# Kernel tuning notes

Hardware: AMD Instinct MI355X
Metric: run time of the kernel (lower is better)

The kernel has to match this reference:

```python
import jax, jax.numpy as jnp
import numpy as np

N_ROWS = 8192
EMBED_DIM = 256


def setup_inputs() -> dict:
    key = jax.random.key(0)
    k1, k2, k3, k4, k5 = jax.random.split(key, 5)
    M = jax.random.normal(k1, (N_ROWS, EMBED_DIM), dtype=jnp.float32)
    N = jax.random.normal(k2, (N_ROWS, EMBED_DIM), dtype=jnp.float32)
    # gate_w: nn.Linear(embed_dim, 1) -> weight [1, d], bias [1]; gate_b extra scalar param [1]
    Wg = jax.random.normal(k3, (1, EMBED_DIM), dtype=jnp.float32) * 0.06
    bg = jax.random.normal(k4, (1,), dtype=jnp.float32) * 0.1
    gate_b = jax.random.normal(k5, (1,), dtype=jnp.float32) * 0.1
    return {"M": M, "N": N, "Wg": Wg, "bg": bg, "gate_b": gate_b, "iseval": 0}


def reference(M, N, Wg, bg, gate_b, iseval):
    # mt: [n, n] cross-similarity scores
    mt = jnp.matmul(N, M.T)
    if not iseval:
        # training branch: zero out the diagonal (mt - diag(diag(mt)))
        n = mt.shape[0]
        idx = jnp.arange(n)
        mt = mt.at[idx, idx].set(0.0)
    else:
        # eval branch: zero out the first row
        mt = mt.at[0].set(0.0)
    attn_weight = jax.nn.softmax(mt, axis=-1)          # [n, n]
    out_attn = jnp.matmul(attn_weight, M)              # [n, d]
    gate = jax.nn.sigmoid(jnp.matmul(out_attn, Wg.T) + bg + gate_b)  # [n, 1]
    boosted = out_attn * gate + N * (1.0 - gate)       # [n, d]
    return boosted[:, None, None, :]                   # [n, 1, 1, d]
```

## Files before the change

### kernel.cpp

```cpp
#include <hip/hip_runtime.h>


constexpr int EMBED = 256;
constexpr int BQ = 64;
constexpr int BJ = 32;
constexpr int NT = 256;

constexpr int SS_OFF = 0;
constexpr int SS_BUF = 18432;
constexpr int PH_OFF = 36864;
constexpr int PH_BUF = 5120;
constexpr int MS_OFF = 47104;
constexpr int LS_OFF = 47360;
constexpr int AS_OFF = 47616;
constexpr int AS_BUF = 256;
constexpr int LDS_SZ = 48128;

typedef _Float16 half8 __attribute__((ext_vector_type(8)));
typedef float f32x4 __attribute__((ext_vector_type(4)));
typedef short short8v __attribute__((ext_vector_type(8)));

static __device__ __forceinline__ f32x4 mfma16(half8 a, half8 b, f32x4 c) {
    return __builtin_amdgcn_mfma_f32_16x16x32_f16(a, b, c, 0, 0, 0);
}
static __device__ __forceinline__ short f2h(float x) {
    return (short)__builtin_bit_cast(unsigned short, (_Float16)x);
}

__global__ void prep(const float* __restrict__ M,
                     short* __restrict__ MhG, short* __restrict__ MtG) {
    __shared__ float L[16 * 260];
    const int r0 = blockIdx.x * 16;
    const int t = threadIdx.x;
    const int pj = t >> 4, pc = (t & 15) * 16;
    {
        const float* src = M + (size_t)(r0 + pj) * EMBED + pc;
        float4 v[4];
        #pragma unroll
        for (int i = 0; i < 4; ++i) v[i] = ((const float4*)src)[i];
        short* hd = MhG + (size_t)(r0 + pj) * EMBED + pc;
        #pragma unroll
        for (int i = 0; i < 2; ++i) {
            float4 a = v[2 * i], b = v[2 * i + 1];
            short8v h;
            h[0]=f2h(a.x); h[1]=f2h(a.y); h[2]=f2h(a.z); h[3]=f2h(a.w);
            h[4]=f2h(b.x); h[5]=f2h(b.y); h[6]=f2h(b.z); h[7]=f2h(b.w);
            *(short8v*)(hd + 8 * i) = h;
        }
        #pragma unroll
        for (int i = 0; i < 4; ++i)
            *(float4*)(L + pj * 260 + pc + 4 * i) = v[i];
    }
    __syncthreads();
    {
        const int d = t;
        const int tile = r0 >> 5, jh = (r0 >> 4) & 1;
        short* dst = MtG + (size_t)tile * (BJ * EMBED) + d * BJ + jh * 16;
        #pragma unroll
        for (int g2 = 0; g2 < 2; ++g2) {
            short8v w;
            #pragma unroll
            for (int e = 0; e < 8; ++e) w[e] = f2h(L[(g2 * 8 + e) * 260 + d]);
            *(short8v*)(dst + g2 * 8) = w;
        }
    }
}

__launch_bounds__(NT, 2)
__global__ void attn(const short* __restrict__ MhG, const short* __restrict__ MtG,
                     const float* __restrict__ Ng, const int* __restrict__ iseval_p,
                     float* __restrict__ O0out, short* __restrict__ Ofp,
                     float* __restrict__ MLm, float* __restrict__ MLl, int n)
{
    __shared__ __align__(16) char smem[LDS_SZ];
    float* MS = (float*)(smem + MS_OFF);
    float* LS = (float*)(smem + LS_OFF);

    const int t = threadIdx.x, lane = t & 63, wave = t >> 6;
    const int quad = lane >> 4, mn = lane & 15;
    const int bid = blockIdx.x;
    const int s  = (bid & 7) >> 1;
    const int qb = ((bid >> 3) << 1) | (bid & 1);
    const int q0 = qb * BQ;
    const int jbase = s * (n >> 2);
    const int jb32 = jbase / BJ;
    const int ntiles = (n >> 2) / BJ;
    const int iseval = *iseval_p;
    const int jt = wave & 1, kh = wave >> 1;
    const int dq = wave;
    const int sq = t >> 2, sh = t & 3;

    if (t < BQ) { MS[t] = -1e30f; LS[t] = 0.f; }

    half8 Qf[4][4];
    #pragma unroll
    for (int qi = 0; qi < 4; ++qi) {
        const float* np = Ng + (size_t)(q0 + qi * 16 + mn) * EMBED;
        #pragma unroll
        for (int kk = 0; kk < 4; ++kk) {
            const float* p = np + (kh * 4 + kk) * 32 + quad * 8;
            float4 a = *(const float4*)p, b = *(const float4*)(p + 4);
            half8 h;
            h[0]=(_Float16)a.x; h[1]=(_Float16)a.y; h[2]=(_Float16)a.z; h[3]=(_Float16)a.w;
            h[4]=(_Float16)b.x; h[5]=(_Float16)b.y; h[6]=(_Float16)b.z; h[7]=(_Float16)b.w;
            Qf[qi][kk] = h;
        }
    }

    f32x4 O[4][4];
    #pragma unroll
    for (int qi = 0; qi < 4; ++qi)
        #pragma unroll
        for (int dt = 0; dt < 4; ++dt) O[qi][dt] = (f32x4){0.f, 0.f, 0.f, 0.f};

    const short* mhb0 = MhG + (size_t)(jbase + jt * 16 + mn) * EMBED + kh * 128 + quad * 8;
    half8 Bc[4], Bn[4], Mtf[4];
    #pragma unroll
    for (int kk = 0; kk < 4; ++kk) Bc[kk] = *(const half8*)(mhb0 + kk * 32);

    for (int tt = 0; tt <= ntiles; ++tt) {
        const int bw = tt & 1;
        const int br = bw ^ 1;

        if (tt > 0) {
            const short* mtb = MtG + (size_t)(jb32 + (tt - 1)) * (BJ * EMBED);
            #pragma unroll
            for (int dt = 0; dt < 4; ++dt)
                Mtf[dt] = *(const half8*)(mtb + (dq * 64 + dt * 16 + mn) * BJ + quad * 8);
        }

        if (tt < ntiles) {
            f32x4 a0 = (f32x4){0,0,0,0}, a1 = (f32x4){0,0,0,0};
            f32x4 a2 = (f32x4){0,0,0,0}, a3 = (f32x4){0,0,0,0};
            #pragma unroll
            for (int kk = 0; kk < 4; ++kk) {
                half8 bf = Bc[kk];
                a0 = mfma16(Qf[0][kk], bf, a0);
                a1 = mfma16(Qf[1][kk], bf, a1);
                a2 = mfma16(Qf[2][kk], bf, a2);
                a3 = mfma16(Qf[3][kk], bf, a3);
            }
            float* ssp = (float*)(smem + SS_OFF + bw * SS_BUF) + kh * 2304;
            #pragma unroll
            for (int r = 0; r < 4; ++r) {
                ssp[(0  + quad * 4 + r) * 36 + jt * 16 + mn] = a0[r];
                ssp[(16 + quad * 4 + r) * 36 + jt * 16 + mn] = a1[r];
                ssp[(32 + quad * 4 + r) * 36 + jt * 16 + mn] = a2[r];
                ssp[(48 + quad * 4 + r) * 36 + jt * 16 + mn] = a3[r];
            }
        }

        if (tt + 1 < ntiles) {
            const short* nb = mhb0 + (size_t)(tt + 1) * (BJ * EMBED);
            #pragma unroll
            for (int kk = 0; kk < 4; ++kk) Bn[kk] = *(const half8*)(nb + kk * 32);
        }

        if (tt > 0) {
            const int j0g = jbase + (tt - 1) * BJ;
            const float* p0 = (const float*)(smem + SS_OFF + br * SS_BUF) + sq * 36 + 8 * sh;
            float4 sa = *(const float4*)p0;
            float4 sb = *(const float4*)(p0 + 4);
            float4 sc = *(const float4*)(p0 + 2304);
            float4 sd = *(const float4*)(p0 + 2308);
            float sv[8] = {sa.x + sc.x, sa.y + sc.y, sa.z + sc.z, sa.w + sc.w,
                           sb.x + sd.x, sb.y + sd.y, sb.z + sd.z, sb.w + sd.w};
            const int qg = q0 + sq;
            if (iseval) {
                if (qg == 0) {
                    #pragma unroll
                    for (int i = 0; i < 8; ++i) sv[i] = 0.f;
                }
            } else {
                int dj = qg - j0g - 8 * sh;
                #pragma unroll
                for (int i = 0; i < 8; ++i) if (dj == i) sv[i] = 0.f;
            }
            float mx = sv[0];
            #pragma unroll
            for (int i = 1; i < 8; ++i) mx = fmaxf(mx, sv[i]);
            mx = fmaxf(mx, __shfl_xor(mx, 1));
            mx = fmaxf(mx, __shfl_xor(mx, 2));
            float m_old = MS[sq];
            float m_new = fmaxf(m_old, mx);
            float alpha = __expf(m_old - m_new);
            float p[8], ps = 0.f;
            #pragma unroll
            for (int i = 0; i < 8; ++i) { p[i] = __expf(sv[i] - m_new); ps += p[i]; }
            ps += __shfl_xor(ps, 1);
            ps += __shfl_xor(ps, 2);
            if (sh == 0) {
                MS[sq] = m_new;
                ((float*)(smem + AS_OFF + br * AS_BUF))[sq] = alpha;
                LS[sq] = LS[sq] * alpha + ps;
            }
            half8 ph;
            #pragma unroll
            for (int i = 0; i < 8; ++i) ph[i] = (_Float16)p[i];
            *(half8*)(smem + PH_OFF + br * PH_BUF + sq * 80 + sh * 16) = ph;
        }

        __syncthreads();

        if (tt > 0) {
            #pragma unroll
            for (int qi = 0; qi < 4; ++qi) {
                half8 pf = *(const half8*)(smem + PH_OFF + br * PH_BUF + (qi * 16 + mn) * 80 + quad * 16);
                f32x4 al = *(const f32x4*)((const float*)(smem + AS_OFF + br * AS_BUF) + qi * 16 + quad * 4);
                #pragma unroll
                for (int dt = 0; dt < 4; ++dt) {
                    f32x4 o = O[qi][dt];
                    o[0] *= al[0]; o[1] *= al[1]; o[2] *= al[2]; o[3] *= al[3];
                    O[qi][dt] = mfma16(pf, Mtf[dt], o);
                }
            }
        }

        #pragma unroll
        for (int kk = 0; kk < 4; ++kk) Bc[kk] = Bn[kk];
    }

    if (s == 0) {
        #pragma unroll
        for (int qi = 0; qi < 4; ++qi)
            #pragma unroll
            for (int dt = 0; dt < 4; ++dt) {
                int col = dq * 64 + dt * 16 + mn;
                #pragma unroll
                for (int r = 0; r < 4; ++r)
                    O0out[(size_t)(q0 + qi * 16 + quad * 4 + r) * EMBED + col] = O[qi][dt][r];
            }
    } else {
        short* dst = Ofp + (size_t)(s - 1) * n * EMBED;
        #pragma unroll
        for (int qi = 0; qi < 4; ++qi)
            #pragma unroll
            for (int dt = 0; dt < 4; ++dt) {
                int col = dq * 64 + dt * 16 + mn;
                #pragma unroll
                for (int r = 0; r < 4; ++r)
                    dst[(size_t)(q0 + qi * 16 + quad * 4 + r) * EMBED + col] = f2h(O[qi][dt][r]);
            }
    }
    if (t < BQ) {
        MLm[s * n + q0 + t] = MS[t];
        MLl[s * n + q0 + t] = LS[t];
    }
}

__global__ void combine4(const float* __restrict__ O0, const short* __restrict__ Ofp,
                         const float* __restrict__ MLm, const float* __restrict__ MLl,
                         const float* __restrict__ Ng, const float* __restrict__ Wg,
                         const float* __restrict__ bg, const float* __restrict__ gb,
                         float* __restrict__ out, int n)
{
    const int t = threadIdx.x;
    const int row = blockIdx.x * 16 + (t >> 4);
    const int c = t & 15;
    float ms[4], ls[4];
    #pragma unroll
    for (int k = 0; k < 4; ++k) { ms[k] = MLm[k * n + row]; ls[k] = MLl[k * n + row]; }
    float m = fmaxf(fmaxf(ms[0], ms[1]), fmaxf(ms[2], ms[3]));
    float w[4], lsum = 0.f;
    #pragma unroll
    for (int k = 0; k < 4; ++k) { w[k] = __expf(ms[k] - m); lsum += w[k] * ls[k]; }
    float linv = 1.f / lsum;

    float acc[16];
    {
        const float4* o0 = (const float4*)(O0 + (size_t)row * EMBED + c * 16);
        #pragma unroll
        for (int i = 0; i < 4; ++i) {
            float4 v = o0[i];
            acc[4*i+0] = w[0] * v.x; acc[4*i+1] = w[0] * v.y;
            acc[4*i+2] = w[0] * v.z; acc[4*i+3] = w[0] * v.w;
        }
    }
    #pragma unroll
    for (int k = 1; k < 4; ++k) {
        const short* op = Ofp + (size_t)(k - 1) * n * EMBED + (size_t)row * EMBED + c * 16;
        half8 a = *(const half8*)op, b = *(const half8*)(op + 8);
        #pragma unroll
        for (int i = 0; i < 8; ++i) {
            acc[i]     += w[k] * (float)a[i];
            acc[8 + i] += w[k] * (float)b[i];
        }
    }
    float dot = 0.f;
    #pragma unroll
    for (int i = 0; i < 16; ++i) { acc[i] *= linv; dot += acc[i] * Wg[c * 16 + i]; }
    dot += __shfl_xor(dot, 1);
    dot += __shfl_xor(dot, 2);
    dot += __shfl_xor(dot, 4);
    dot += __shfl_xor(dot, 8);
    float g = 1.f / (1.f + __expf(-(dot + bg[0] + gb[0])));
    const float4* n4 = (const float4*)(Ng + (size_t)row * EMBED + c * 16);
    float4* o4 = (float4*)(out + (size_t)row * EMBED + c * 16);
    #pragma unroll
    for (int i = 0; i < 4; ++i) {
        float4 nn = n4[i];
        float4 res;
        res.x = acc[4*i+0] * g + nn.x * (1.f - g);
        res.y = acc[4*i+1] * g + nn.y * (1.f - g);
        res.z = acc[4*i+2] * g + nn.z * (1.f - g);
        res.w = acc[4*i+3] * g + nn.w * (1.f - g);
        o4[i] = res;
    }
}

extern "C" void kernel_launch(void* const* d_in, const int* in_sizes, int n_in,
                              void* d_out, int out_size, void* d_ws, size_t ws_size,
                              hipStream_t stream) {
    const float* M      = (const float*)d_in[0];
    const float* N      = (const float*)d_in[1];
    const float* Wgp    = (const float*)d_in[2];
    const float* bgp    = (const float*)d_in[3];
    const float* gbp    = (const float*)d_in[4];
    const int*   iseval = (const int*)d_in[5];
    float* out = (float*)d_out;

    int n = in_sizes[0] / EMBED;
    short* MhG = (short*)d_ws;
    short* MtG = MhG + (size_t)n * EMBED;
    short* Ofp = MtG + (size_t)n * EMBED;
    float* MLm = (float*)(Ofp + (size_t)3 * n * EMBED);
    float* MLl = MLm + 4 * n;

    hipLaunchKernelGGL(prep, dim3(n / 16), dim3(NT), 0, stream, M, MhG, MtG);
    hipLaunchKernelGGL(attn, dim3((n / BQ) * 4), dim3(NT), 0, stream,
                       MhG, MtG, N, iseval, out, Ofp, MLm, MLl, n);
    hipLaunchKernelGGL(combine4, dim3(n / 16), dim3(NT), 0, stream,
                       out, Ofp, MLm, MLl, N, Wgp, bgp, gbp, out, n);
}
```

Measured before the change: 185.3 us.

## Split QK^T across query halves instead of K halves, keep softmax stats in registers

Each wave now computes full-K dot products for half of the query rows (2 q-tiles × 8 k-chunks) instead of half the K dimension for all 4 q-tiles. This removes the partial-sum buffer and the second pair of LDS reads and adds in the softmax stage, halving the score scratch in LDS. Running max and sum move from LDS into per-thread registers, which drops shared-memory traffic and the sh==0 stores. The trade-off is more B-fragment registers per wave (8 half8 for Bc/Bn plus 16 for Qf), which may raise register pressure against the two-blocks-per-SIMD launch bound.

After: 240.4 us. 1.3x slower.

```diff
diff --git a/kernel.cpp b/kernel.cpp
--- a/kernel.cpp
+++ b/kernel.cpp
@@ -7,14 +7,12 @@
 constexpr int NT = 256;
 
 constexpr int SS_OFF = 0;
-constexpr int SS_BUF = 18432;
-constexpr int PH_OFF = 36864;
+constexpr int SS_BUF = 9216;
+constexpr int PH_OFF = 18432;
 constexpr int PH_BUF = 5120;
-constexpr int MS_OFF = 47104;
-constexpr int LS_OFF = 47360;
-constexpr int AS_OFF = 47616;
+constexpr int AS_OFF = 28672;
 constexpr int AS_BUF = 256;
-constexpr int LDS_SZ = 48128;
+constexpr int LDS_SZ = 29184;
 
 typedef _Float16 half8 __attribute__((ext_vector_type(8)));
 typedef float f32x4 __attribute__((ext_vector_type(4)));
@@ -73,8 +71,6 @@
                      float* __restrict__ MLm, float* __restrict__ MLl, int n)
 {
     __shared__ __align__(16) char smem[LDS_SZ];
-    float* MS = (float*)(smem + MS_OFF);
-    float* LS = (float*)(smem + LS_OFF);
 
     const int t = threadIdx.x, lane = t & 63, wave = t >> 6;
     const int quad = lane >> 4, mn = lane & 15;
@@ -86,19 +82,17 @@
     const int jb32 = jbase / BJ;
     const int ntiles = (n >> 2) / BJ;
     const int iseval = *iseval_p;
-    const int jt = wave & 1, kh = wave >> 1;
+    const int jt = wave & 1, qh = wave >> 1;
     const int dq = wave;
     const int sq = t >> 2, sh = t & 3;
 
-    if (t < BQ) { MS[t] = -1e30f; LS[t] = 0.f; }
-
-    half8 Qf[4][4];
-    #pragma unroll
-    for (int qi = 0; qi < 4; ++qi) {
-        const float* np = Ng + (size_t)(q0 + qi * 16 + mn) * EMBED;
-        #pragma unroll
-        for (int kk = 0; kk < 4; ++kk) {
-            const float* p = np + (kh * 4 + kk) * 32 + quad * 8;
+    half8 Qf[2][8];
+    #pragma unroll
+    for (int qi = 0; qi < 2; ++qi) {
+        const float* np = Ng + (size_t)(q0 + (qh * 2 + qi) * 16 + mn) * EMBED;
+        #pragma unroll
+        for (int kk = 0; kk < 8; ++kk) {
+            const float* p = np + kk * 32 + quad * 8;
             float4 a = *(const float4*)p, b = *(const float4*)(p + 4);
             half8 h;
             h[0]=(_Float16)a.x; h[1]=(_Float16)a.y; h[2]=(_Float16)a.z; h[3]=(_Float16)a.w;
@@ -113,10 +107,12 @@
         #pragma unroll
         for (int dt = 0; dt < 4; ++dt) O[qi][dt] = (f32x4){0.f, 0.f, 0.f, 0.f};
 
-    const short* mhb0 = MhG + (size_t)(jbase + jt * 16 + mn) * EMBED + kh * 128 + quad * 8;
-    half8 Bc[4], Bn[4], Mtf[4];
-    #pragma unroll
-    for (int kk = 0; kk < 4; ++kk) Bc[kk] = *(const half8*)(mhb0 + kk * 32);
+    const short* mhb0 = MhG + (size_t)(jbase + jt * 16 + mn) * EMBED + quad * 8;
+    half8 Bc[8], Bn[8], Mtf[4];
+    #pragma unroll
+    for (int kk = 0; kk < 8; ++kk) Bc[kk] = *(const half8*)(mhb0 + kk * 32);
+
+    float m_reg = -1e30f, l_reg = 0.f;
 
     for (int tt = 0; tt <= ntiles; ++tt) {
         const int bw = tt & 1;
@@ -131,29 +127,25 @@
 
         if (tt < ntiles) {
             f32x4 a0 = (f32x4){0,0,0,0}, a1 = (f32x4){0,0,0,0};
-            f32x4 a2 = (f32x4){0,0,0,0}, a3 = (f32x4){0,0,0,0};
-            #pragma unroll
-            for (int kk = 0; kk < 4; ++kk) {
+            #pragma unroll
+            for (int kk = 0; kk < 8; ++kk) {
                 half8 bf = Bc[kk];
                 a0 = mfma16(Qf[0][kk], bf, a0);
                 a1 = mfma16(Qf[1][kk], bf, a1);
-                a2 = mfma16(Qf[2][kk], bf, a2);
-                a3 = mfma16(Qf[3][kk], bf, a3);
-            }
-            float* ssp = (float*)(smem + SS_OFF + bw * SS_BUF) + kh * 2304;
+            }
+            float* ssp = (float*)(smem + SS_OFF + bw * SS_BUF);
+            const int rb = qh * 32;
             #pragma unroll
             for (int r = 0; r < 4; ++r) {
-                ssp[(0  + quad * 4 + r) * 36 + jt * 16 + mn] = a0[r];
-                ssp[(16 + quad * 4 + r) * 36 + jt * 16 + mn] = a1[r];
-                ssp[(32 + quad * 4 + r) * 36 + jt * 16 + mn] = a2[r];
-                ssp[(48 + quad * 4 + r) * 36 + jt * 16 + mn] = a3[r];
+                ssp[(rb +      quad * 4 + r) * 36 + jt * 16 + mn] = a0[r];
+                ssp[(rb + 16 + quad * 4 + r) * 36 + jt * 16 + mn] = a1[r];
             }
         }
 
         if (tt + 1 < ntiles) {
             const short* nb = mhb0 + (size_t)(tt + 1) * (BJ * EMBED);
             #pragma unroll
-            for (int kk = 0; kk < 4; ++kk) Bn[kk] = *(const half8*)(nb + kk * 32);
+            for (int kk = 0; kk < 8; ++kk) Bn[kk] = *(const half8*)(nb + kk * 32);
         }
 
         if (tt > 0) {
@@ -161,10 +153,7 @@
             const float* p0 = (const float*)(smem + SS_OFF + br * SS_BUF) + sq * 36 + 8 * sh;
             float4 sa = *(const float4*)p0;
             float4 sb = *(const float4*)(p0 + 4);
-            float4 sc = *(const float4*)(p0 + 2304);
-            float4 sd = *(const float4*)(p0 + 2308);
-            float sv[8] = {sa.x + sc.x, sa.y + sc.y, sa.z + sc.z, sa.w + sc.w,
-                           sb.x + sd.x, sb.y + sd.y, sb.z + sd.z, sb.w + sd.w};
+            float sv[8] = {sa.x, sa.y, sa.z, sa.w, sb.x, sb.y, sb.z, sb.w};
             const int qg = q0 + sq;
             if (iseval) {
                 if (qg == 0) {
@@ -181,19 +170,17 @@
             for (int i = 1; i < 8; ++i) mx = fmaxf(mx, sv[i]);
             mx = fmaxf(mx, __shfl_xor(mx, 1));
             mx = fmaxf(mx, __shfl_xor(mx, 2));
-            float m_old = MS[sq];
-            float m_new = fmaxf(m_old, mx);
-            float alpha = __expf(m_old - m_new);
+            float m_new = fmaxf(m_reg, mx);
+            float alpha = __expf(m_reg - m_new);
             float p[8], ps = 0.f;
             #pragma unroll
             for (int i = 0; i < 8; ++i) { p[i] = __expf(sv[i] - m_new); ps += p[i]; }
             ps += __shfl_xor(ps, 1);
             ps += __shfl_xor(ps, 2);
-            if (sh == 0) {
-                MS[sq] = m_new;
+            m_reg = m_new;
+            l_reg = l_reg * alpha + ps;
+            if (sh == 0)
                 ((float*)(smem + AS_OFF + br * AS_BUF))[sq] = alpha;
-                LS[sq] = LS[sq] * alpha + ps;
-            }
             half8 ph;
             #pragma unroll
             for (int i = 0; i < 8; ++i) ph[i] = (_Float16)p[i];
@@ -217,7 +204,7 @@
         }
 
         #pragma unroll
-        for (int kk = 0; kk < 4; ++kk) Bc[kk] = Bn[kk];
+        for (int kk = 0; kk < 8; ++kk) Bc[kk] = Bn[kk];
     }
 
     if (s == 0) {
@@ -242,9 +229,9 @@
                     dst[(size_t)(q0 + qi * 16 + quad * 4 + r) * EMBED + col] = f2h(O[qi][dt][r]);
             }
     }
-    if (t < BQ) {
-        MLm[s * n + q0 + t] = MS[t];
-        MLl[s * n + q0 + t] = LS[t];
+    if (sh == 0) {
+        MLm[s * n + q0 + sq] = m_reg;
+        MLl[s * n + q0 + sq] = l_reg;
     }
 }
 
```

## Use lazy softmax rescaling with exp2 and register-held row statistics

Applied to the files above, without the earlier changes.

Pre-scales Q by log2(e) so the softmax can use exp2 directly, and keeps the running max and sum in registers instead of LDS. The running max is only raised when a new tile exceeds it by more than 8, and a block-wide flag tells the PV stage whether any row needs its O accumulator rescaled, so most tiles skip the alpha multiplies. It also raises wave priority around the MFMA sections. The lazy threshold lets exp2 values grow up to 2^8 before rescaling, which reduces fp16 headroom for P; scores far below the max also round to zero.

New measurement: 200.6 us. 8.2% more time.

```diff
diff --git a/kernel.cpp b/kernel.cpp
--- a/kernel.cpp
+++ b/kernel.cpp
@@ -10,11 +10,10 @@
 constexpr int SS_BUF = 18432;
 constexpr int PH_OFF = 36864;
 constexpr int PH_BUF = 5120;
-constexpr int MS_OFF = 47104;
-constexpr int LS_OFF = 47360;
-constexpr int AS_OFF = 47616;
+constexpr int AS_OFF = 47104;
 constexpr int AS_BUF = 256;
-constexpr int LDS_SZ = 48128;
+constexpr int FL_OFF = 47616;
+constexpr int LDS_SZ = 47648;
 
 typedef _Float16 half8 __attribute__((ext_vector_type(8)));
 typedef float f32x4 __attribute__((ext_vector_type(4)));
@@ -73,8 +72,6 @@
                      float* __restrict__ MLm, float* __restrict__ MLl, int n)
 {
     __shared__ __align__(16) char smem[LDS_SZ];
-    float* MS = (float*)(smem + MS_OFF);
-    float* LS = (float*)(smem + LS_OFF);
 
     const int t = threadIdx.x, lane = t & 63, wave = t >> 6;
     const int quad = lane >> 4, mn = lane & 15;
@@ -90,8 +87,9 @@
     const int dq = wave;
     const int sq = t >> 2, sh = t & 3;
 
-    if (t < BQ) { MS[t] = -1e30f; LS[t] = 0.f; }
-
+    if (t < 2) ((int*)(smem + FL_OFF))[t] = -1;
+
+    const float L2E = 1.4426950408889634f;
     half8 Qf[4][4];
     #pragma unroll
     for (int qi = 0; qi < 4; ++qi) {
@@ -101,8 +99,10 @@
             const float* p = np + (kh * 4 + kk) * 32 + quad * 8;
             float4 a = *(const float4*)p, b = *(const float4*)(p + 4);
             half8 h;
-            h[0]=(_Float16)a.x; h[1]=(_Float16)a.y; h[2]=(_Float16)a.z; h[3]=(_Float16)a.w;
-            h[4]=(_Float16)b.x; h[5]=(_Float16)b.y; h[6]=(_Float16)b.z; h[7]=(_Float16)b.w;
+            h[0]=(_Float16)(a.x*L2E); h[1]=(_Float16)(a.y*L2E);
+            h[2]=(_Float16)(a.z*L2E); h[3]=(_Float16)(a.w*L2E);
+            h[4]=(_Float16)(b.x*L2E); h[5]=(_Float16)(b.y*L2E);
+            h[6]=(_Float16)(b.z*L2E); h[7]=(_Float16)(b.w*L2E);
             Qf[qi][kk] = h;
         }
     }
@@ -112,11 +112,15 @@
     for (int qi = 0; qi < 4; ++qi)
         #pragma unroll
         for (int dt = 0; dt < 4; ++dt) O[qi][dt] = (f32x4){0.f, 0.f, 0.f, 0.f};
+
+    float m_reg = -1e30f, l_reg = 0.f;
 
     const short* mhb0 = MhG + (size_t)(jbase + jt * 16 + mn) * EMBED + kh * 128 + quad * 8;
     half8 Bc[4], Bn[4], Mtf[4];
     #pragma unroll
     for (int kk = 0; kk < 4; ++kk) Bc[kk] = *(const half8*)(mhb0 + kk * 32);
+
+    __syncthreads();
 
     for (int tt = 0; tt <= ntiles; ++tt) {
         const int bw = tt & 1;
@@ -132,6 +136,7 @@
         if (tt < ntiles) {
             f32x4 a0 = (f32x4){0,0,0,0}, a1 = (f32x4){0,0,0,0};
             f32x4 a2 = (f32x4){0,0,0,0}, a3 = (f32x4){0,0,0,0};
+            __builtin_amdgcn_s_setprio(1);
             #pragma unroll
             for (int kk = 0; kk < 4; ++kk) {
                 half8 bf = Bc[kk];
@@ -140,6 +145,7 @@
                 a2 = mfma16(Qf[2][kk], bf, a2);
                 a3 = mfma16(Qf[3][kk], bf, a3);
             }
+            __builtin_amdgcn_s_setprio(0);
             float* ssp = (float*)(smem + SS_OFF + bw * SS_BUF) + kh * 2304;
             #pragma unroll
             for (int r = 0; r < 4; ++r) {
@@ -157,7 +163,8 @@
         }
 
         if (tt > 0) {
-            const int j0g = jbase + (tt - 1) * BJ;
+            const int stamp = tt - 1;
+            const int j0g = jbase + stamp * BJ;
             const float* p0 = (const float*)(smem + SS_OFF + br * SS_BUF) + sq * 36 + 8 * sh;
             float4 sa = *(const float4*)p0;
             float4 sb = *(const float4*)(p0 + 4);
@@ -181,19 +188,22 @@
             for (int i = 1; i < 8; ++i) mx = fmaxf(mx, sv[i]);
             mx = fmaxf(mx, __shfl_xor(mx, 1));
             mx = fmaxf(mx, __shfl_xor(mx, 2));
-            float m_old = MS[sq];
-            float m_new = fmaxf(m_old, mx);
-            float alpha = __expf(m_old - m_new);
+            float alpha = 1.f;
+            bool need = (mx > m_reg + 8.f);
+            if (need) {
+                alpha = exp2f(m_reg - mx);
+                m_reg = mx;
+            }
             float p[8], ps = 0.f;
             #pragma unroll
-            for (int i = 0; i < 8; ++i) { p[i] = __expf(sv[i] - m_new); ps += p[i]; }
+            for (int i = 0; i < 8; ++i) { p[i] = exp2f(sv[i] - m_reg); ps += p[i]; }
             ps += __shfl_xor(ps, 1);
             ps += __shfl_xor(ps, 2);
-            if (sh == 0) {
-                MS[sq] = m_new;
+            l_reg = l_reg * alpha + ps;
+            if (sh == 0)
                 ((float*)(smem + AS_OFF + br * AS_BUF))[sq] = alpha;
-                LS[sq] = LS[sq] * alpha + ps;
-            }
+            if (need)
+                ((int*)(smem + FL_OFF))[br] = stamp;
             half8 ph;
             #pragma unroll
             for (int i = 0; i < 8; ++i) ph[i] = (_Float16)p[i];
@@ -203,17 +213,26 @@
         __syncthreads();
 
         if (tt > 0) {
+            const bool resc = (((const int*)(smem + FL_OFF))[br] == tt - 1);
+            __builtin_amdgcn_s_setprio(1);
             #pragma unroll
             for (int qi = 0; qi < 4; ++qi) {
                 half8 pf = *(const half8*)(smem + PH_OFF + br * PH_BUF + (qi * 16 + mn) * 80 + quad * 16);
-                f32x4 al = *(const f32x4*)((const float*)(smem + AS_OFF + br * AS_BUF) + qi * 16 + quad * 4);
-                #pragma unroll
-                for (int dt = 0; dt < 4; ++dt) {
-                    f32x4 o = O[qi][dt];
-                    o[0] *= al[0]; o[1] *= al[1]; o[2] *= al[2]; o[3] *= al[3];
-                    O[qi][dt] = mfma16(pf, Mtf[dt], o);
+                if (resc) {
+                    f32x4 al = *(const f32x4*)((const float*)(smem + AS_OFF + br * AS_BUF) + qi * 16 + quad * 4);
+                    #pragma unroll
+                    for (int dt = 0; dt < 4; ++dt) {
+                        f32x4 o = O[qi][dt];
+                        o[0] *= al[0]; o[1] *= al[1]; o[2] *= al[2]; o[3] *= al[3];
+                        O[qi][dt] = mfma16(pf, Mtf[dt], o);
+                    }
+                } else {
+                    #pragma unroll
+                    for (int dt = 0; dt < 4; ++dt)
+                        O[qi][dt] = mfma16(pf, Mtf[dt], O[qi][dt]);
                 }
             }
+            __builtin_amdgcn_s_setprio(0);
         }
 
         #pragma unroll
@@ -242,9 +261,9 @@
                     dst[(size_t)(q0 + qi * 16 + quad * 4 + r) * EMBED + col] = f2h(O[qi][dt][r]);
             }
     }
-    if (t < BQ) {
-        MLm[s * n + q0 + t] = MS[t];
-        MLl[s * n + q0 + t] = LS[t];
+    if (sh == 0) {
+        MLm[s * n + q0 + sq] = m_reg;
+        MLl[s * n + q0 + sq] = l_reg;
     }
 }
 
@@ -263,7 +282,7 @@
     float m = fmaxf(fmaxf(ms[0], ms[1]), fmaxf(ms[2], ms[3]));
     float w[4], lsum = 0.f;
     #pragma unroll
-    for (int k = 0; k < 4; ++k) { w[k] = __expf(ms[k] - m); lsum += w[k] * ls[k]; }
+    for (int k = 0; k < 4; ++k) { w[k] = exp2f(ms[k] - m); lsum += w[k] * ls[k]; }
     float linv = 1.f / lsum;
 
     float acc[16];
```
